# Kernel tuning notes

Hardware: AMD Instinct MI355X
Metric: run time of the kernel (lower is better)

The kernel has to match this reference:

```python
import jax, jax.numpy as jnp
import numpy as np

EPS = 1e-8
N_CLASSES = 11


def _instance_loss(views_1, views_2, masks, labels):
    # views_*: [1, C, H, W]; masks: [1, K, H, W] binary; labels: [1, K] in [0,11)
    C = views_1.shape[1]
    X1 = views_1[0].reshape(C, -1)                      # [C, P]
    X2 = views_2[0].reshape(C, -1)                      # [C, P]
    K = masks.shape[1]
    M = (masks[0].reshape(K, -1) == 1).astype(X1.dtype) # [K, P]
    lab = labels[0]                                     # [K]

    counts = M.sum(axis=1)                              # [K] pixels per instance
    cnt = jnp.maximum(counts, 1.0)

    # per-instance mean feature vector over masked view-1 pixels
    per_chan_sum = M @ X1.T                             # [K, C]
    means = per_chan_sum / cnt[:, None]                 # [K, C]

    # torch.std over ALL elements of the gathered [N_k, C] block (unbiased)
    n_elem = counts * C                                 # [K]
    sum_all = per_chan_sum.sum(axis=1)                  # [K]
    mean_all = sum_all / jnp.maximum(n_elem, 1.0)
    sumsq = M @ (X1 * X1).sum(axis=0)                   # [K]
    var = (sumsq - n_elem * mean_all * mean_all) / jnp.maximum(n_elem - 1.0, 1.0)
    std = jnp.sqrt(jnp.maximum(var, 0.0))               # [K]

    # pairwise mean cosine sim: sim[i,j] = mean_{p in mask_j} cos(means[i], X2[:,p])
    norm_m = jnp.sqrt((means * means).sum(axis=1))      # [K]
    norm_2 = jnp.sqrt((X2 * X2).sum(axis=0))            # [P]
    D = means @ X2                                      # [K, P]
    ratio = D / jnp.maximum(norm_m[:, None] * norm_2[None, :], EPS)
    sim = (ratio @ M.T) / cnt[None, :]                  # [K, K]

    same = lab[:, None] == lab[None, :]
    eye = jnp.eye(K, dtype=bool)

    instance_sim = jnp.zeros(N_CLASSES, X1.dtype).at[lab].add(jnp.diagonal(sim))
    class_sim = jnp.zeros(N_CLASSES, X1.dtype).at[lab].add(
        jnp.where(same & ~eye, sim, 0.0).sum(axis=1))
    class_std = jnp.zeros(N_CLASSES, X1.dtype).at[lab].add(std)

    # negative-pair buckets: human={1,2}, 4wheel={3..8}, 2wheel={9,10}
    g_hum_4w = (lab >= 1) & (lab <= 8)                  # human or 4wheel
    g_4w_2w = (lab >= 3) & (lab <= 10)                  # 4wheel or 2wheel
    g_hum_2w = ((lab >= 1) & (lab <= 2)) | ((lab >= 9) & (lab <= 10))
    diff = ~same

    def neg_bucket(g):
        pair = diff & g[:, None] & g[None, :]
        c = pair.sum().astype(X1.dtype)
        s = jnp.where(pair, sim, 0.0).sum()
        return jnp.where(c > 1, s / c, s).reshape(1)

    neg_4w_hum = neg_bucket(g_hum_4w)
    neg_4w_2w = neg_bucket(g_4w_2w)
    neg_hum_2w = neg_bucket(g_hum_2w)

    class_counts = jnp.zeros(N_CLASSES, X1.dtype).at[lab].add(1.0)
    many = class_counts > 1
    instance_sim = jnp.where(many, instance_sim / jnp.maximum(class_counts, 1.0), instance_sim)
    class_sim = jnp.where(
        many, class_sim / jnp.maximum(class_counts * (class_counts - 1.0), 1.0), class_sim)
    class_std = jnp.where(many, class_std / jnp.maximum(class_counts, 1.0), class_std)

    return instance_sim, class_sim, neg_4w_hum, neg_4w_2w, neg_hum_2w, class_std


def setup_inputs() -> dict:
    key = jax.random.key(0)
    k1, k2, k3, k4 = jax.random.split(key, 4)
    views_1 = jax.random.normal(k1, (1, 64, 512, 512), dtype=jnp.float32)
    views_2 = jax.random.normal(k2, (1, 64, 512, 512), dtype=jnp.float32)
    masks = jax.random.randint(k3, (1, 16, 512, 512), 0, 2, dtype=jnp.int32)
    labels = jax.random.randint(k4, (1, 16), 0, 11, dtype=jnp.int32)
    return {"views_1": views_1, "views_2": views_2, "masks": masks, "labels": labels}


def reference(views_1, views_2, masks, labels):
    return _instance_loss(views_1, views_2, masks, labels)
```

## Files before the change

### kernel.cpp

```cpp
#include <hip/hip_runtime.h>

#define PIX 262144
#define CCH 64
#define KK  16

typedef __attribute__((ext_vector_type(8))) short short8;
typedef __attribute__((ext_vector_type(4))) float f32x4;

__global__ __launch_bounds__(256) void k1_fused(
        const int* __restrict__ masks, const float* __restrict__ x2,
        unsigned short* __restrict__ packed, float* __restrict__ counts_s,
        float* __restrict__ yv) {
    __shared__ float wc[4][16];
    if (blockIdx.x < 512) {
        int t = blockIdx.x * 256 + threadIdx.x;
        int p = t * 2;
        unsigned m0 = 0, m1 = 0;
        #pragma unroll
        for (int k = 0; k < KK; ++k) {
            int2 mv = *(const int2*)(masks + (size_t)k * PIX + p);
            m0 |= (unsigned)(mv.x == 1) << k;
            m1 |= (unsigned)(mv.y == 1) << k;
        }
        packed[p]     = (unsigned short)m0;
        packed[p + 1] = (unsigned short)m1;

        int wid = threadIdx.x >> 6, lane = threadIdx.x & 63;
        #pragma unroll
        for (int k = 0; k < KK; ++k) {
            unsigned long long b0 = __ballot((m0 >> k) & 1u);
            unsigned long long b1 = __ballot((m1 >> k) & 1u);
            if (lane == 0) wc[wid][k] = (float)(__popcll(b0) + __popcll(b1));
        }
        __syncthreads();
        if (threadIdx.x < 16) {
            int k = threadIdx.x;
            float s = wc[0][k] + wc[1][k] + wc[2][k] + wc[3][k];
            atomicAdd(counts_s + k * 32 + (blockIdx.x & 31), s);
        }
    } else {
        int b2 = blockIdx.x - 512;
        int p = (b2 * 256 + threadIdx.x) * 2;
        float s0 = 0.f, s1 = 0.f;
        #pragma unroll 16
        for (int c = 0; c < CCH; ++c) {
            float2 v = *(const float2*)(x2 + (size_t)c * PIX + p);
            s0 = fmaf(v.x, v.x, s0);
            s1 = fmaf(v.y, v.y, s1);
        }
        float2 y;
        y.x = (s0 > 0.f) ? rsqrtf(s0) : 0.f;
        y.y = (s1 > 0.f) ? rsqrtf(s1) : 0.f;
        *(float2*)(yv + p) = y;
    }
}

__device__ __forceinline__ float wred64(float v) {
    #pragma unroll
    for (int o = 32; o > 0; o >>= 1) v += __shfl_xor(v, o, 64);
    return v;
}

__global__ __launch_bounds__(256) void k2_mfma(
        const float* __restrict__ x1, const float* __restrict__ x2,
        const unsigned short* __restrict__ packed, const float* __restrict__ yv,
        float* __restrict__ psum_c, float* __restrict__ psumsq_c,
        float* __restrict__ G_c) {
    int b = blockIdx.x;
    bool TB = (b >= 2048);
    if (TB) b -= 2048;
    int lane = threadIdx.x & 63;
    int wv   = threadIdx.x >> 6;
    int quad = lane >> 4;
    int n    = lane & 15;
    int ch   = wv * 16 + n;
    int base = b * 128;
    int cp   = b & 31;

    const float* Xrow = (TB ? x2 : x1) + (size_t)ch * PIX;

    int4 pk[4]; float4 xa[4], xb[4], ya[4], yb[4];
    #pragma unroll
    for (int i = 0; i < 4; ++i) {
        int kof = base + i * 32 + (quad << 3);
        pk[i] = *(const int4*)(packed + kof);
        xa[i] = *(const float4*)(Xrow + kof);
        xb[i] = *(const float4*)(Xrow + kof + 4);
    }
    if (TB) {
        #pragma unroll
        for (int i = 0; i < 4; ++i) {
            int kof = base + i * 32 + (quad << 3);
            ya[i] = *(const float4*)(yv + kof);
            yb[i] = *(const float4*)(yv + kof + 4);
        }
    }

    f32x4 acc0 = {0.f, 0.f, 0.f, 0.f};
    f32x4 acc1 = {0.f, 0.f, 0.f, 0.f};
    const short ONE = (short)0x3F80;

    #pragma unroll
    for (int i = 0; i < 4; ++i) {
        short8 af;
        af[0] = ((pk[i].x >> n) & 1)        ? ONE : (short)0;
        af[1] = ((pk[i].x >> (n + 16)) & 1) ? ONE : (short)0;
        af[2] = ((pk[i].y >> n) & 1)        ? ONE : (short)0;
        af[3] = ((pk[i].y >> (n + 16)) & 1) ? ONE : (short)0;
        af[4] = ((pk[i].z >> n) & 1)        ? ONE : (short)0;
        af[5] = ((pk[i].z >> (n + 16)) & 1) ? ONE : (short)0;
        af[6] = ((pk[i].w >> n) & 1)        ? ONE : (short)0;
        af[7] = ((pk[i].w >> (n + 16)) & 1) ? ONE : (short)0;

        float xs[8] = {xa[i].x, xa[i].y, xa[i].z, xa[i].w,
                       xb[i].x, xb[i].y, xb[i].z, xb[i].w};
        if (TB) {
            float ys[8] = {ya[i].x, ya[i].y, ya[i].z, ya[i].w,
                           yb[i].x, yb[i].y, yb[i].z, yb[i].w};
            #pragma unroll
            for (int j = 0; j < 8; ++j) xs[j] *= ys[j];
        }

        short8 bh, bl;
        #pragma unroll
        for (int j = 0; j < 8; ++j) {
            unsigned u = __float_as_uint(xs[j]);
            bh[j] = (short)(u >> 16);
            float hi = __uint_as_float(u & 0xFFFF0000u);
            bl[j] = (short)(__float_as_uint(xs[j] - hi) >> 16);
        }
        acc0 = __builtin_amdgcn_mfma_f32_16x16x32_bf16(af, bh, acc0, 0, 0, 0);
        acc0 = __builtin_amdgcn_mfma_f32_16x16x32_bf16(af, bl, acc0, 0, 0, 0);

        if (!TB) {
            short8 qh, ql;
            #pragma unroll
            for (int j = 0; j < 8; ++j) {
                float sq = xs[j] * xs[j];
                unsigned u = __float_as_uint(sq);
                qh[j] = (short)(u >> 16);
                float hi = __uint_as_float(u & 0xFFFF0000u);
                ql[j] = (short)(__float_as_uint(sq - hi) >> 16);
            }
            acc1 = __builtin_amdgcn_mfma_f32_16x16x32_bf16(af, qh, acc1, 0, 0, 0);
            acc1 = __builtin_amdgcn_mfma_f32_16x16x32_bf16(af, ql, acc1, 0, 0, 0);
        }
    }

    int col = wv * 16 + n;
    #pragma unroll
    for (int r = 0; r < 4; ++r) {
        int idx = cp * 1024 + (quad * 4 + r) * 64 + col;
        if (TB) {
            atomicAdd(G_c + idx, acc0[r]);
        } else {
            atomicAdd(psum_c + idx, acc0[r]);
            atomicAdd(psumsq_c + idx, acc1[r]);
        }
    }
}

__global__ __launch_bounds__(256) void k3_finalize(
        const int* __restrict__ labels, const float* __restrict__ counts_s,
        const float* __restrict__ psum_c, const float* __restrict__ psumsq_c,
        const float* __restrict__ G_c, float* __restrict__ out) {
    __shared__ float meansS[16][65];
    __shared__ float Gs[16][65];
    __shared__ float cntS[16], rawcS[16], nmS[16], stdS[16], rowS[16];
    __shared__ float ssq2[16][17];
    __shared__ float ssqS[16];
    __shared__ int   labS[16];
    __shared__ float simS[16][17];
    __shared__ float bred[4][6];
    int t = threadIdx.x;

    if (t < 16) {
        float s = 0.f;
        #pragma unroll 8
        for (int j = 0; j < 32; ++j) s += counts_s[t * 32 + j];
        rawcS[t] = s;
        cntS[t]  = fmaxf(s, 1.f);
        labS[t]  = labels[t];
    }
    {
        int k = t >> 4, seg = t & 15;
        float s = 0.f;
        for (int cp = 0; cp < 32; ++cp) {
            const float4 v = *(const float4*)(psumsq_c + cp * 1024 + k * 64 + seg * 4);
            s += v.x + v.y + v.z + v.w;
        }
        ssq2[k][seg] = s;
    }
    __syncthreads();
    if (t < 16) {
        float s = 0.f;
        #pragma unroll
        for (int seg = 0; seg < 16; ++seg) s += ssq2[t][seg];
        ssqS[t] = s;
    }
    for (int i = t; i < 1024; i += 256) {
        int k = i >> 6, c = i & 63;
        float sp = 0.f, sg = 0.f;
        #pragma unroll 8
        for (int cp = 0; cp < 32; ++cp) {
            sp += psum_c[cp * 1024 + i];
            sg += G_c[cp * 1024 + i];
        }
        meansS[k][c] = sp / cntS[k];
        Gs[k][c] = sg;
    }
    __syncthreads();
    if (t < 16) {
        float s2 = 0.f, sm = 0.f;
        for (int c = 0; c < 64; ++c) {
            float m = meansS[t][c];
            s2 = fmaf(m, m, s2);
            sm += m;
        }
        nmS[t] = sqrtf(s2);
        float ne = rawcS[t] * 64.f;
        float ma = (sm * cntS[t]) / fmaxf(ne, 1.f);
        float var = (ssqS[t] - ne * ma * ma) / fmaxf(ne - 1.f, 1.f);
        stdS[t] = sqrtf(fmaxf(var, 0.f));
    }
    __syncthreads();
    {
        int i = t >> 4, j = t & 15;
        float d = 0.f;
        #pragma unroll 16
        for (int c = 0; c < 64; ++c) d = fmaf(meansS[i][c], Gs[j][c], d);
        simS[i][j] = d / (fmaxf(nmS[i], 1e-30f) * cntS[j]);
    }
    __syncthreads();
    if (t < 16) {
        float s = 0.f;
        int li = labS[t];
        for (int j = 0; j < 16; ++j)
            if (j != t && labS[j] == li) s += simS[t][j];
        rowS[t] = s;
    }
    float s0 = 0.f, s1 = 0.f, s2 = 0.f, c0 = 0.f, c1 = 0.f, c2 = 0.f;
    {
        int i = t >> 4, j = t & 15;
        int li = labS[i], lj = labS[j];
        if (li != lj) {
            float sv = simS[i][j];
            bool gi0 = li >= 1 && li <= 8,  gj0 = lj >= 1 && lj <= 8;
            bool gi1 = li >= 3 && li <= 10, gj1 = lj >= 3 && lj <= 10;
            bool gi2 = (li >= 1 && li <= 2) || (li >= 9 && li <= 10);
            bool gj2 = (lj >= 1 && lj <= 2) || (lj >= 9 && lj <= 10);
            if (gi0 && gj0) { s0 = sv; c0 = 1.f; }
            if (gi1 && gj1) { s1 = sv; c1 = 1.f; }
            if (gi2 && gj2) { s2 = sv; c2 = 1.f; }
        }
    }
    s0 = wred64(s0); s1 = wred64(s1); s2 = wred64(s2);
    c0 = wred64(c0); c1 = wred64(c1); c2 = wred64(c2);
    {
        int wid = t >> 6, lane = t & 63;
        if (lane == 0) {
            bred[wid][0] = s0; bred[wid][1] = s1; bred[wid][2] = s2;
            bred[wid][3] = c0; bred[wid][4] = c1; bred[wid][5] = c2;
        }
    }
    __syncthreads();
    if (t < 11) {
        float cc = 0.f, inst = 0.f, csim = 0.f, cstd = 0.f;
        for (int k = 0; k < 16; ++k) {
            if (labS[k] == t) {
                cc += 1.f;
                inst += simS[k][k];
                csim += rowS[k];
                cstd += stdS[k];
            }
        }
        if (cc > 1.f) {
            inst /= fmaxf(cc, 1.f);
            csim /= fmaxf(cc * (cc - 1.f), 1.f);
            cstd /= cc;
        }
        out[t]      = inst;
        out[11 + t] = csim;
        out[25 + t] = cstd;
    }
    if (t == 0) {
        float S0 = bred[0][0] + bred[1][0] + bred[2][0] + bred[3][0];
        float S1 = bred[0][1] + bred[1][1] + bred[2][1] + bred[3][1];
        float S2 = bred[0][2] + bred[1][2] + bred[2][2] + bred[3][2];
        float C0 = bred[0][3] + bred[1][3] + bred[2][3] + bred[3][3];
        float C1 = bred[0][4] + bred[1][4] + bred[2][4] + bred[3][4];
        float C2 = bred[0][5] + bred[1][5] + bred[2][5] + bred[3][5];
        out[22] = (C0 > 1.f) ? (S0 / C0) : S0;
        out[23] = (C1 > 1.f) ? (S1 / C1) : S1;
        out[24] = (C2 > 1.f) ? (S2 / C2) : S2;
    }
}

extern "C" void kernel_launch(void* const* d_in, const int* in_sizes, int n_in,
                              void* d_out, int out_size, void* d_ws, size_t ws_size,
                              hipStream_t stream) {
    const float* x1     = (const float*)d_in[0];
    const float* x2     = (const float*)d_in[1];
    const int*   masks  = (const int*)d_in[2];
    const int*   labels = (const int*)d_in[3];
    float* out = (float*)d_out;

    char* ws = (char*)d_ws;
    unsigned short* packed = (unsigned short*)ws;
    float* yv       = (float*)(ws + (size_t)PIX * 2);
    float* counts_s = (float*)(ws + (size_t)PIX * 6);
    float* psum_c   = counts_s + 512;
    float* psumsq_c = psum_c + 32 * 1024;
    float* G_c      = psumsq_c + 32 * 1024;

    hipMemsetAsync(counts_s, 0, (512 + 3 * 32 * 1024) * sizeof(float), stream);
    k1_fused<<<1024, 256, 0, stream>>>(masks, x2, packed, counts_s, yv);
    k2_mfma<<<4096, 256, 0, stream>>>(x1, x2, packed, yv, psum_c, psumsq_c, G_c);
    k3_finalize<<<1, 256, 0, stream>>>(labels, counts_s, psum_c, psumsq_c, G_c, out);
}
```

Before: 202.0 us.

## Fuse mask packing and x2 norm computation into the MFMA kernel

Removes the separate preprocessing kernel that packed masks into bitfields and computed per-pixel inverse norms of view 2. The main MFMA kernel now reads the raw int32 masks directly, and blocks working on view 2 compute the per-pixel channel norm through a shuffle reduction plus shared-memory reduction across the four waves. Mask counts are accumulated by wave 0 of the view-1 blocks. This saves one launch and the packed/yv round trip through memory. In exchange, each block reads the full int32 masks twice (once per view branch), which is more traffic than the packed 16-bit form, and a __syncthreads is added to the view-2 path.

Result: no change. 202.8 us (+0.4%).

```diff
diff --git a/kernel.cpp b/kernel.cpp
--- a/kernel.cpp
+++ b/kernel.cpp
@@ -7,65 +7,18 @@
 typedef __attribute__((ext_vector_type(8))) short short8;
 typedef __attribute__((ext_vector_type(4))) float f32x4;
 
-__global__ __launch_bounds__(256) void k1_fused(
-        const int* __restrict__ masks, const float* __restrict__ x2,
-        unsigned short* __restrict__ packed, float* __restrict__ counts_s,
-        float* __restrict__ yv) {
-    __shared__ float wc[4][16];
-    if (blockIdx.x < 512) {
-        int t = blockIdx.x * 256 + threadIdx.x;
-        int p = t * 2;
-        unsigned m0 = 0, m1 = 0;
-        #pragma unroll
-        for (int k = 0; k < KK; ++k) {
-            int2 mv = *(const int2*)(masks + (size_t)k * PIX + p);
-            m0 |= (unsigned)(mv.x == 1) << k;
-            m1 |= (unsigned)(mv.y == 1) << k;
-        }
-        packed[p]     = (unsigned short)m0;
-        packed[p + 1] = (unsigned short)m1;
-
-        int wid = threadIdx.x >> 6, lane = threadIdx.x & 63;
-        #pragma unroll
-        for (int k = 0; k < KK; ++k) {
-            unsigned long long b0 = __ballot((m0 >> k) & 1u);
-            unsigned long long b1 = __ballot((m1 >> k) & 1u);
-            if (lane == 0) wc[wid][k] = (float)(__popcll(b0) + __popcll(b1));
-        }
-        __syncthreads();
-        if (threadIdx.x < 16) {
-            int k = threadIdx.x;
-            float s = wc[0][k] + wc[1][k] + wc[2][k] + wc[3][k];
-            atomicAdd(counts_s + k * 32 + (blockIdx.x & 31), s);
-        }
-    } else {
-        int b2 = blockIdx.x - 512;
-        int p = (b2 * 256 + threadIdx.x) * 2;
-        float s0 = 0.f, s1 = 0.f;
-        #pragma unroll 16
-        for (int c = 0; c < CCH; ++c) {
-            float2 v = *(const float2*)(x2 + (size_t)c * PIX + p);
-            s0 = fmaf(v.x, v.x, s0);
-            s1 = fmaf(v.y, v.y, s1);
-        }
-        float2 y;
-        y.x = (s0 > 0.f) ? rsqrtf(s0) : 0.f;
-        y.y = (s1 > 0.f) ? rsqrtf(s1) : 0.f;
-        *(float2*)(yv + p) = y;
-    }
-}
-
 __device__ __forceinline__ float wred64(float v) {
     #pragma unroll
     for (int o = 32; o > 0; o >>= 1) v += __shfl_xor(v, o, 64);
     return v;
 }
 
-__global__ __launch_bounds__(256) void k2_mfma(
+__global__ __launch_bounds__(256) void k2_all(
         const float* __restrict__ x1, const float* __restrict__ x2,
-        const unsigned short* __restrict__ packed, const float* __restrict__ yv,
+        const int* __restrict__ masks, float* __restrict__ counts_s,
         float* __restrict__ psum_c, float* __restrict__ psumsq_c,
         float* __restrict__ G_c) {
+    __shared__ float ylds[128][4];
     int b = blockIdx.x;
     bool TB = (b >= 2048);
     if (TB) b -= 2048;
@@ -78,22 +31,62 @@
     int cp   = b & 31;
 
     const float* Xrow = (TB ? x2 : x1) + (size_t)ch * PIX;
-
-    int4 pk[4]; float4 xa[4], xb[4], ya[4], yb[4];
+    const int*   Mrow = masks + (size_t)n * PIX;
+
+    int4 mk[8]; float4 xa[4], xb[4];
     #pragma unroll
     for (int i = 0; i < 4; ++i) {
         int kof = base + i * 32 + (quad << 3);
-        pk[i] = *(const int4*)(packed + kof);
+        mk[2*i]   = *(const int4*)(Mrow + kof);
+        mk[2*i+1] = *(const int4*)(Mrow + kof + 4);
         xa[i] = *(const float4*)(Xrow + kof);
         xb[i] = *(const float4*)(Xrow + kof + 4);
     }
+
+    float xs[4][8], sq[4][8];
+    #pragma unroll
+    for (int i = 0; i < 4; ++i) {
+        xs[i][0]=xa[i].x; xs[i][1]=xa[i].y; xs[i][2]=xa[i].z; xs[i][3]=xa[i].w;
+        xs[i][4]=xb[i].x; xs[i][5]=xb[i].y; xs[i][6]=xb[i].z; xs[i][7]=xb[i].w;
+        #pragma unroll
+        for (int j = 0; j < 8; ++j) sq[i][j] = xs[i][j] * xs[i][j];
+    }
+
     if (TB) {
         #pragma unroll
-        for (int i = 0; i < 4; ++i) {
-            int kof = base + i * 32 + (quad << 3);
-            ya[i] = *(const float4*)(yv + kof);
-            yb[i] = *(const float4*)(yv + kof + 4);
-        }
+        for (int off = 1; off < 16; off <<= 1)
+            #pragma unroll
+            for (int i = 0; i < 4; ++i)
+                #pragma unroll
+                for (int j = 0; j < 8; ++j)
+                    sq[i][j] += __shfl_xor(sq[i][j], off, 64);
+        if (n == 0) {
+            #pragma unroll
+            for (int i = 0; i < 4; ++i)
+                #pragma unroll
+                for (int j = 0; j < 8; ++j)
+                    ylds[i * 32 + (quad << 3) + j][wv] = sq[i][j];
+        }
+        __syncthreads();
+        #pragma unroll
+        for (int i = 0; i < 4; ++i)
+            #pragma unroll
+            for (int j = 0; j < 8; ++j) {
+                float4 v = *(const float4*)ylds[i * 32 + (quad << 3) + j];
+                float s = v.x + v.y + v.z + v.w;
+                float y = (s > 0.f) ? rsqrtf(s) : 0.f;
+                xs[i][j] *= y;
+            }
+    } else if (wv == 0) {
+        int cnt = 0;
+        #pragma unroll
+        for (int i = 0; i < 8; ++i) {
+            cnt += (mk[i].x == 1) + (mk[i].y == 1) + (mk[i].z == 1) + (mk[i].w == 1);
+        }
+        float fc = (float)cnt;
+        fc += __shfl_xor(fc, 16, 64);
+        fc += __shfl_xor(fc, 32, 64);
+        if (quad == 0) atomicAdd(counts_s + n * 32 + cp, fc);
     }
 
     f32x4 acc0 = {0.f, 0.f, 0.f, 0.f};
@@ -103,31 +96,23 @@
     #pragma unroll
     for (int i = 0; i < 4; ++i) {
         short8 af;
-        af[0] = ((pk[i].x >> n) & 1)        ? ONE : (short)0;
-        af[1] = ((pk[i].x >> (n + 16)) & 1) ? ONE : (short)0;
-        af[2] = ((pk[i].y >> n) & 1)        ? ONE : (short)0;
-        af[3] = ((pk[i].y >> (n + 16)) & 1) ? ONE : (short)0;
-        af[4] = ((pk[i].z >> n) & 1)        ? ONE : (short)0;
-        af[5] = ((pk[i].z >> (n + 16)) & 1) ? ONE : (short)0;
-        af[6] = ((pk[i].w >> n) & 1)        ? ONE : (short)0;
-        af[7] = ((pk[i].w >> (n + 16)) & 1) ? ONE : (short)0;
-
-        float xs[8] = {xa[i].x, xa[i].y, xa[i].z, xa[i].w,
-                       xb[i].x, xb[i].y, xb[i].z, xb[i].w};
-        if (TB) {
-            float ys[8] = {ya[i].x, ya[i].y, ya[i].z, ya[i].w,
-                           yb[i].x, yb[i].y, yb[i].z, yb[i].w};
-            #pragma unroll
-            for (int j = 0; j < 8; ++j) xs[j] *= ys[j];
-        }
+        af[0] = (mk[2*i].x   == 1) ? ONE : (short)0;
+        af[1] = (mk[2*i].y   == 1) ? ONE : (short)0;
+        af[2] = (mk[2*i].z   == 1) ? ONE : (short)0;
+        af[3] = (mk[2*i].w   == 1) ? ONE : (short)0;
+        af[4] = (mk[2*i+1].x == 1) ? ONE : (short)0;
+        af[5] = (mk[2*i+1].y == 1) ? ONE : (short)0;
+        af[6] = (mk[2*i+1].z == 1) ? ONE : (short)0;
+        af[7] = (mk[2*i+1].w == 1) ? ONE : (short)0;
 
         short8 bh, bl;
         #pragma unroll
         for (int j = 0; j < 8; ++j) {
-            unsigned u = __float_as_uint(xs[j]);
+            float v = xs[i][j];
+            unsigned u = __float_as_uint(v);
             bh[j] = (short)(u >> 16);
             float hi = __uint_as_float(u & 0xFFFF0000u);
-            bl[j] = (short)(__float_as_uint(xs[j] - hi) >> 16);
+            bl[j] = (short)(__float_as_uint(v - hi) >> 16);
         }
         acc0 = __builtin_amdgcn_mfma_f32_16x16x32_bf16(af, bh, acc0, 0, 0, 0);
         acc0 = __builtin_amdgcn_mfma_f32_16x16x32_bf16(af, bl, acc0, 0, 0, 0);
@@ -136,11 +121,11 @@
             short8 qh, ql;
             #pragma unroll
             for (int j = 0; j < 8; ++j) {
-                float sq = xs[j] * xs[j];
-                unsigned u = __float_as_uint(sq);
+                float v = sq[i][j];
+                unsigned u = __float_as_uint(v);
                 qh[j] = (short)(u >> 16);
                 float hi = __uint_as_float(u & 0xFFFF0000u);
-                ql[j] = (short)(__float_as_uint(sq - hi) >> 16);
+                ql[j] = (short)(__float_as_uint(v - hi) >> 16);
             }
             acc1 = __builtin_amdgcn_mfma_f32_16x16x32_bf16(af, qh, acc1, 0, 0, 0);
             acc1 = __builtin_amdgcn_mfma_f32_16x16x32_bf16(af, ql, acc1, 0, 0, 0);
@@ -305,16 +290,13 @@
     const int*   labels = (const int*)d_in[3];
     float* out = (float*)d_out;
 
-    char* ws = (char*)d_ws;
-    unsigned short* packed = (unsigned short*)ws;
-    float* yv       = (float*)(ws + (size_t)PIX * 2);
-    float* counts_s = (float*)(ws + (size_t)PIX * 6);
+    float* ws = (float*)d_ws;
+    float* counts_s = ws;
     float* psum_c   = counts_s + 512;
     float* psumsq_c = psum_c + 32 * 1024;
     float* G_c      = psumsq_c + 32 * 1024;
 
     hipMemsetAsync(counts_s, 0, (512 + 3 * 32 * 1024) * sizeof(float), stream);
-    k1_fused<<<1024, 256, 0, stream>>>(masks, x2, packed, counts_s, yv);
-    k2_mfma<<<4096, 256, 0, stream>>>(x1, x2, packed, yv, psum_c, psumsq_c, G_c);
+    k2_all<<<4096, 256, 0, stream>>>(x1, x2, masks, counts_s, psum_c, psumsq_c, G_c);
     k3_finalize<<<1, 256, 0, stream>>>(labels, counts_s, psum_c, psumsq_c, G_c, out);
 }
```
